# Performance work log

Measured on AMD Instinct MI355X. Metric: run time of the kernel, lower is better.

The kernel has to match this reference:

```python
import jax, jax.numpy as jnp
import numpy as np

DIM = 3072
HEADS = 24
HEAD_DIM = 128
INNER = HEADS * HEAD_DIM
EPS = 1e-6
B, IMG_LEN, TXT_LEN = 1, 2048, 512
S = IMG_LEN + TXT_LEN


def setup_inputs() -> dict:
    key = jax.random.key(0)
    ks = jax.random.split(key, 16)
    w = lambda k, shp: (jax.random.normal(k, shp, dtype=jnp.float32) * 0.02)
    return {
        "x": jax.random.normal(ks[0], (B, IMG_LEN, DIM), dtype=jnp.float32),
        "ctx": jax.random.normal(ks[1], (B, TXT_LEN, DIM), dtype=jnp.float32),
        "rope_cos": jax.random.uniform(ks[2], (S, HEAD_DIM), dtype=jnp.float32),
        "rope_sin": jax.random.uniform(ks[3], (S, HEAD_DIM), dtype=jnp.float32),
        "wq": w(ks[4], (INNER, DIM)),
        "wk": w(ks[5], (INNER, DIM)),
        "wv": w(ks[6], (INNER, DIM)),
        "gq": jnp.ones((HEAD_DIM,), jnp.float32),
        "gk": jnp.ones((HEAD_DIM,), jnp.float32),
        "wo": w(ks[7], (DIM, INNER)),
        "awq": w(ks[8], (INNER, DIM)),
        "awk": w(ks[9], (INNER, DIM)),
        "awv": w(ks[10], (INNER, DIM)),
        "agq": jnp.ones((HEAD_DIM,), jnp.float32),
        "agk": jnp.ones((HEAD_DIM,), jnp.float32),
        "awo": w(ks[11], (DIM, INNER)),
    }


def _rms_norm(t, g):
    # t: [b, s, h, d]; normalize over last dim
    var = jnp.mean(t * t, axis=-1, keepdims=True)
    return t * jax.lax.rsqrt(var + EPS) * g


def _heads(t):
    # [b, s, h*d] -> [b, s, h, d]
    b, s, _ = t.shape
    return t.reshape(b, s, HEADS, HEAD_DIM)


def _apply_rope(t, cos, sin):
    # t: [b, s, h, d]; cos/sin: [s, d] interleaved-pair layout (diffusers Flux style)
    b, s, h, d = t.shape
    x = t.reshape(b, s, h, d // 2, 2)
    rot = jnp.stack([-x[..., 1], x[..., 0]], axis=-1).reshape(b, s, h, d)
    c = cos[None, :, None, :]
    si = sin[None, :, None, :]
    return t * c + rot * si


def reference(x, ctx, rope_cos, rope_sin, wq, wk, wv, gq, gk, wo,
              awq, awk, awv, agq, agk, awo):
    # image-stream QKV + per-head RMSNorm on q,k
    q = _rms_norm(_heads(x @ wq.T), gq)
    k = _rms_norm(_heads(x @ wk.T), gk)
    v = _heads(x @ wv.T)
    # context-stream QKV
    qc = _rms_norm(_heads(ctx @ awq.T), agq)
    kc = _rms_norm(_heads(ctx @ awk.T), agk)
    vc = _heads(ctx @ awv.T)
    # joint streams: [ctx, img] ordering (out[:, :txt_len] is context)
    q = jnp.concatenate([qc, q], axis=1)
    k = jnp.concatenate([kc, k], axis=1)
    v = jnp.concatenate([vc, v], axis=1)
    q = _apply_rope(q, rope_cos, rope_sin)
    k = _apply_rope(k, rope_cos, rope_sin)
    # SDPA
    scale = 1.0 / jnp.sqrt(jnp.float32(HEAD_DIM))
    scores = jnp.einsum('bqhd,bkhd->bhqk', q, k) * scale
    probs = jax.nn.softmax(scores, axis=-1)
    out = jnp.einsum('bhqk,bkhd->bqhd', probs, v)
    out = out.reshape(out.shape[0], out.shape[1], INNER)
    img_out = out[:, TXT_LEN:] @ wo.T
    txt_out = out[:, :TXT_LEN] @ awo.T
    return (img_out, txt_out)
```

## Files before the change

kernel.cpp:

```cpp
#include <hip/hip_runtime.h>
#include <hip/hip_bf16.h>

#define DIMC 3072
#define NHEADS 24
#define HD 128
#define SEQ 2560
#define TXTLEN 512
#define IMGLEN 2048

using short8 = __attribute__((ext_vector_type(8))) short;
using f32x4  = __attribute__((ext_vector_type(4))) float;

static __device__ __forceinline__ float bf2f(unsigned short u) {
    unsigned v = ((unsigned)u) << 16;
    return __builtin_bit_cast(float, v);
}
static __device__ __forceinline__ unsigned short f2bf(float f) {
    unsigned u = __builtin_bit_cast(unsigned, f);
    return (unsigned short)((u + 0x7FFFu + ((u >> 16) & 1u)) >> 16);
}
static __device__ __forceinline__ void gload16(const void* g, void* l) {
    __builtin_amdgcn_global_load_lds((const __attribute__((address_space(1))) unsigned int*)g,
                                     (__attribute__((address_space(3))) unsigned int*)l,
                                     16, 0, 0);
}

__global__ __launch_bounds__(256)
void castk(const float* __restrict__ in, unsigned short* __restrict__ out, int n8)
{
    const int i = blockIdx.x * 256 + threadIdx.x;
    if (i >= n8) return;
    const float4 a = *reinterpret_cast<const float4*>(in + (size_t)i * 8);
    const float4 b = *reinterpret_cast<const float4*>(in + (size_t)i * 8 + 4);
    short8 o;
    o[0] = (short)f2bf(a.x); o[1] = (short)f2bf(a.y);
    o[2] = (short)f2bf(a.z); o[3] = (short)f2bf(a.w);
    o[4] = (short)f2bf(b.x); o[5] = (short)f2bf(b.y);
    o[6] = (short)f2bf(b.z); o[7] = (short)f2bf(b.w);
    *reinterpret_cast<short8*>(out + (size_t)i * 8) = o;
}

struct W8 { const float* src[8]; };
__global__ __launch_bounds__(256)
void castw(W8 a, unsigned short* __restrict__ dstbase, int n8, size_t wsz)
{
    const int i = blockIdx.x * 256 + threadIdx.x;
    if (i >= n8) return;
    const float* in = a.src[blockIdx.y];
    unsigned short* out = dstbase + (size_t)blockIdx.y * wsz;
    const float4 av = *reinterpret_cast<const float4*>(in + (size_t)i * 8);
    const float4 bv = *reinterpret_cast<const float4*>(in + (size_t)i * 8 + 4);
    short8 o;
    o[0] = (short)f2bf(av.x); o[1] = (short)f2bf(av.y);
    o[2] = (short)f2bf(av.z); o[3] = (short)f2bf(av.w);
    o[4] = (short)f2bf(bv.x); o[5] = (short)f2bf(bv.y);
    o[6] = (short)f2bf(bv.z); o[7] = (short)f2bf(bv.w);
    *reinterpret_cast<short8*>(out + (size_t)i * 8) = o;
}

struct QkvArgs {
    const unsigned short* A;
    const unsigned short* w0[3];
    const unsigned short* w1[3];
    unsigned short* c[3];
};

__global__ __launch_bounds__(256)
void gemm_qkv(QkvArgs args)
{
    __shared__ unsigned short As[2][128 * 32];
    __shared__ unsigned short Bs[2][128 * 32];

    const int bid = blockIdx.x;
    const int swz = (bid & 7) * 180 + (bid >> 3);
    const int bm = swz % 20;
    int bn = swz / 20;
    const int which = bn / 24; bn -= which * 24;

    const int rowbase = bm * 128, colbase = bn * 128;
    const unsigned short* __restrict__ A = args.A;
    const unsigned short* __restrict__ W = (rowbase < TXTLEN) ? args.w0[which] : args.w1[which];
    unsigned short* __restrict__ C = args.c[which];

    const int t = threadIdx.x, w = t >> 6, l = t & 63;
    const int lr = l & 15, lk = l >> 4;
    const int wr = (w >> 1) * 64, wc = (w & 1) * 64;

    f32x4 acc[4][4] = {};

    const unsigned short* Ag = A + (size_t)(rowbase + w * 32 + (l >> 2)) * DIMC + (l & 3) * 8;
    const unsigned short* Wg = W + (size_t)(colbase + w * 32 + (l >> 2)) * DIMC + (l & 3) * 8;

    auto STAGE = [&](int buf, int k0) {
        gload16(Ag + k0,             &As[buf][w * 1024]);
        gload16(Ag + 16 * DIMC + k0, &As[buf][w * 1024 + 512]);
        gload16(Wg + k0,             &Bs[buf][w * 1024]);
        gload16(Wg + 16 * DIMC + k0, &Bs[buf][w * 1024 + 512]);
    };

    STAGE(0, 0);

    constexpr int NIT = DIMC / 32;
    for (int it = 0; it < NIT; ++it) {
        const int buf = it & 1;
        __syncthreads();
        if (it + 1 < NIT) STAGE(buf ^ 1, (it + 1) * 32);

        short8 af[4], bf[4];
#pragma unroll
        for (int m = 0; m < 4; ++m)
            af[m] = *reinterpret_cast<const short8*>(&As[buf][(wr + m * 16 + lr) * 32 + lk * 8]);
#pragma unroll
        for (int n = 0; n < 4; ++n)
            bf[n] = *reinterpret_cast<const short8*>(&Bs[buf][(wc + n * 16 + lr) * 32 + lk * 8]);
#pragma unroll
        for (int m = 0; m < 4; ++m)
#pragma unroll
            for (int n = 0; n < 4; ++n)
                acc[m][n] = __builtin_amdgcn_mfma_f32_16x16x32_bf16(af[m], bf[n], acc[m][n], 0, 0, 0);
    }

#pragma unroll
    for (int m = 0; m < 4; ++m) {
#pragma unroll
        for (int r = 0; r < 4; ++r) {
            const int row = rowbase + wr + m * 16 + lk * 4 + r;
            unsigned short* crow = C + (size_t)row * DIMC + colbase + wc;
#pragma unroll
            for (int n = 0; n < 4; ++n)
                crow[n * 16 + lr] = f2bf(acc[m][n][r]);
        }
    }
}

__global__ __launch_bounds__(256)
void gemm_out(const unsigned short* __restrict__ A, const unsigned short* __restrict__ W0,
              const unsigned short* __restrict__ W1, float* __restrict__ Ctxt,
              float* __restrict__ Cimg)
{
    __shared__ unsigned short As[2][128 * 32];
    __shared__ unsigned short Bs[2][128 * 32];

    const int bid = blockIdx.x;
    const int swz = (bid & 7) * 60 + (bid >> 3);
    const int bm = swz % 20;
    const int bn = swz / 20;

    const int rowbase = bm * 128, colbase = bn * 128;
    const unsigned short* __restrict__ W = (rowbase < TXTLEN) ? W0 : W1;

    const int t = threadIdx.x, w = t >> 6, l = t & 63;
    const int lr = l & 15, lk = l >> 4;
    const int wr = (w >> 1) * 64, wc = (w & 1) * 64;

    f32x4 acc[4][4] = {};

    const unsigned short* Ag = A + (size_t)(rowbase + w * 32 + (l >> 2)) * DIMC + (l & 3) * 8;
    const unsigned short* Wg = W + (size_t)(colbase + w * 32 + (l >> 2)) * DIMC + (l & 3) * 8;

    auto STAGE = [&](int buf, int k0) {
        gload16(Ag + k0,             &As[buf][w * 1024]);
        gload16(Ag + 16 * DIMC + k0, &As[buf][w * 1024 + 512]);
        gload16(Wg + k0,             &Bs[buf][w * 1024]);
        gload16(Wg + 16 * DIMC + k0, &Bs[buf][w * 1024 + 512]);
    };

    STAGE(0, 0);

    constexpr int NIT = DIMC / 32;
    for (int it = 0; it < NIT; ++it) {
        const int buf = it & 1;
        __syncthreads();
        if (it + 1 < NIT) STAGE(buf ^ 1, (it + 1) * 32);

        short8 af[4], bf[4];
#pragma unroll
        for (int m = 0; m < 4; ++m)
            af[m] = *reinterpret_cast<const short8*>(&As[buf][(wr + m * 16 + lr) * 32 + lk * 8]);
#pragma unroll
        for (int n = 0; n < 4; ++n)
            bf[n] = *reinterpret_cast<const short8*>(&Bs[buf][(wc + n * 16 + lr) * 32 + lk * 8]);
#pragma unroll
        for (int m = 0; m < 4; ++m)
#pragma unroll
            for (int n = 0; n < 4; ++n)
                acc[m][n] = __builtin_amdgcn_mfma_f32_16x16x32_bf16(af[m], bf[n], acc[m][n], 0, 0, 0);
    }

    float* Cb; int rloc;
    if (rowbase < TXTLEN) { Cb = Ctxt; rloc = rowbase; }
    else                  { Cb = Cimg; rloc = rowbase - TXTLEN; }
#pragma unroll
    for (int m = 0; m < 4; ++m) {
#pragma unroll
        for (int r = 0; r < 4; ++r) {
            const int row = rloc + wr + m * 16 + lk * 4 + r;
            float* crow = Cb + (size_t)row * DIMC + colbase + wc;
#pragma unroll
            for (int n = 0; n < 4; ++n)
                crow[n * 16 + lr] = acc[m][n][r];
        }
    }
}

__global__ __launch_bounds__(256)
void normrope(unsigned short* __restrict__ Q, unsigned short* __restrict__ K,
              const float* __restrict__ gq, const float* __restrict__ gk,
              const float* __restrict__ agq, const float* __restrict__ agk,
              const float* __restrict__ rc, const float* __restrict__ rs)
{
    const int wid  = (blockIdx.x << 2) + (threadIdx.x >> 6);
    const int lane = threadIdx.x & 63;
    const int s = wid / NHEADS, h = wid - s * NHEADS;
    const bool img = (s >= TXTLEN);
    const float* gq_ = img ? gq : agq;
    const float* gk_ = img ? gk : agk;

    const size_t base = (size_t)s * DIMC + h * HD + lane * 2;
    const float2 c2  = *reinterpret_cast<const float2*>(rc + (size_t)s * HD + lane * 2);
    const float2 s2  = *reinterpret_cast<const float2*>(rs + (size_t)s * HD + lane * 2);
    const float2 gqv = *reinterpret_cast<const float2*>(gq_ + lane * 2);
    const float2 gkv = *reinterpret_cast<const float2*>(gk_ + lane * 2);

    {
        unsigned pr = *reinterpret_cast<unsigned*>(Q + base);
        float vx = bf2f((unsigned short)(pr & 0xffff));
        float vy = bf2f((unsigned short)(pr >> 16));
        float ss = vx * vx + vy * vy;
#pragma unroll
        for (int off = 1; off < 64; off <<= 1) ss += __shfl_xor(ss, off);
        const float rr = rsqrtf(ss * (1.f / HD) + 1e-6f);
        const float txv = vx * rr * gqv.x, tyv = vy * rr * gqv.y;
        const float qs = 0.08838834764831845f;
        const float ox = (txv * c2.x - tyv * s2.x) * qs;
        const float oy = (tyv * c2.y + txv * s2.y) * qs;
        *reinterpret_cast<unsigned*>(Q + base) = (unsigned)f2bf(ox) | ((unsigned)f2bf(oy) << 16);
    }
    {
        unsigned pr = *reinterpret_cast<unsigned*>(K + base);
        float vx = bf2f((unsigned short)(pr & 0xffff));
        float vy = bf2f((unsigned short)(pr >> 16));
        float ss = vx * vx + vy * vy;
#pragma unroll
        for (int off = 1; off < 64; off <<= 1) ss += __shfl_xor(ss, off);
        const float rr = rsqrtf(ss * (1.f / HD) + 1e-6f);
        const float txv = vx * rr * gkv.x, tyv = vy * rr * gkv.y;
        const float ox = txv * c2.x - tyv * s2.x;
        const float oy = tyv * c2.y + txv * s2.y;
        *reinterpret_cast<unsigned*>(K + base) = (unsigned)f2bf(ox) | ((unsigned)f2bf(oy) << 16);
    }
}

__global__ __launch_bounds__(256)
void transpose_v(const unsigned short* __restrict__ V, unsigned short* __restrict__ Vt)
{
    __shared__ unsigned short Ts[64][136];
    const int kt = blockIdx.x, h = blockIdx.y;
    const int t = threadIdx.x;
#pragma unroll
    for (int p = 0; p < 4; ++p) {
        const int row = p * 16 + (t >> 4);
        const int col = (t & 15) * 8;
        *reinterpret_cast<short8*>(&Ts[row][col]) =
            *reinterpret_cast<const short8*>(V + (size_t)(kt * 64 + row) * DIMC + h * HD + col);
    }
    __syncthreads();
    const int d = t >> 1, kh = t & 1;
    unsigned short* dst = Vt + (size_t)h * HD * SEQ + (size_t)d * SEQ + kt * 64 + kh * 32;
#pragma unroll
    for (int j4 = 0; j4 < 4; ++j4) {
        short8 o;
#pragma unroll
        for (int j = 0; j < 8; ++j) o[j] = (short)Ts[kh * 32 + j4 * 8 + j][d];
        *reinterpret_cast<short8*>(dst + j4 * 8) = o;
    }
}

__global__ __launch_bounds__(512)
void attn_mfma(const unsigned short* __restrict__ Q, const unsigned short* __restrict__ K,
               const unsigned short* __restrict__ Vt, unsigned short* __restrict__ O)
{
    __shared__ unsigned short Ks[2][64 * 128];
    __shared__ unsigned short Vs[2][128 * 64];
    __shared__ unsigned short Ps[8][16 * 64];

    const int bq = blockIdx.x, h = blockIdx.y;
    const int t = threadIdx.x, w = t >> 6, l = t & 63;
    const int lr = l & 15, lk = l >> 4;
    const int q0 = bq * 128 + w * 16;

    short8 qf[4];
#pragma unroll
    for (int kk = 0; kk < 4; ++kk)
        qf[kk] = *reinterpret_cast<const short8*>(
            Q + (size_t)(q0 + lr) * DIMC + h * HD + kk * 32 + lk * 8);

    f32x4 oacc[8] = {};
    float mrow[4] = {-1e30f, -1e30f, -1e30f, -1e30f};
    float lrow[4] = {};

    const unsigned short* Kg[2];
    const unsigned short* Vg[2];
#pragma unroll
    for (int i = 0; i < 2; ++i) {
        const int kr = w * 8 + i * 4 + (l >> 4);
        Kg[i] = K + (size_t)kr * DIMC + h * HD + (((l & 15) ^ (kr & 7)) * 8);
        const int vr = w * 16 + i * 8 + (l >> 3);
        Vg[i] = Vt + (size_t)h * HD * SEQ + (size_t)vr * SEQ + (((l & 7) ^ (vr & 7)) * 8);
    }

    auto STAGE = [&](int buf, int kv0) {
#pragma unroll
        for (int i = 0; i < 2; ++i) {
            gload16(Kg[i] + (size_t)kv0 * DIMC, &Ks[buf][(w * 8 + i * 4) * 128]);
            gload16(Vg[i] + kv0,                &Vs[buf][(w * 16 + i * 8) * 64]);
        }
    };

    STAGE(0, 0);

    constexpr int NT = SEQ / 64;
    for (int kt = 0; kt < NT; ++kt) {
        const int buf = kt & 1;
        __syncthreads();
        if (kt + 1 < NT) STAGE(buf ^ 1, (kt + 1) * 64);

        f32x4 sf[4] = {};
        __builtin_amdgcn_s_setprio(1);
#pragma unroll
        for (int nf = 0; nf < 4; ++nf) {
            const int row = nf * 16 + lr;
            const int sw = (row & 7) << 3;
#pragma unroll
            for (int kk = 0; kk < 4; ++kk) {
                short8 bfr = *reinterpret_cast<const short8*>(
                    &Ks[buf][row * 128 + ((kk * 32 + lk * 8) ^ sw)]);
                sf[nf] = __builtin_amdgcn_mfma_f32_16x16x32_bf16(qf[kk], bfr, sf[nf], 0, 0, 0);
            }
        }
        __builtin_amdgcn_s_setprio(0);

        float alpha[4];
#pragma unroll
        for (int r = 0; r < 4; ++r) {
            float mx = fmaxf(fmaxf(sf[0][r], sf[1][r]), fmaxf(sf[2][r], sf[3][r]));
#pragma unroll
            for (int off = 1; off < 16; off <<= 1) mx = fmaxf(mx, __shfl_xor(mx, off));
            const float mn = fmaxf(mrow[r], mx);
            alpha[r] = __expf(mrow[r] - mn);
            mrow[r] = mn;
            float ps = 0.f;
#pragma unroll
            for (int nf = 0; nf < 4; ++nf) {
                const float p = __expf(sf[nf][r] - mn);
                sf[nf][r] = p;
                ps += p;
            }
#pragma unroll
            for (int off = 1; off < 16; off <<= 1) ps += __shfl_xor(ps, off);
            lrow[r] = lrow[r] * alpha[r] + ps;
        }
#pragma unroll
        for (int nf = 0; nf < 8; ++nf)
#pragma unroll
            for (int r = 0; r < 4; ++r) oacc[nf][r] *= alpha[r];

#pragma unroll
        for (int r = 0; r < 4; ++r) {
            const int prow = lk * 4 + r;
            const int sw = (prow & 7) << 3;
#pragma unroll
            for (int nf = 0; nf < 4; ++nf) {
                const int col = nf * 16 + lr;
                Ps[w][prow * 64 + (col ^ sw)] = f2bf(sf[nf][r]);
            }
        }

        __builtin_amdgcn_s_setprio(1);
#pragma unroll
        for (int ks = 0; ks < 2; ++ks) {
            short8 pa = *reinterpret_cast<const short8*>(
                &Ps[w][lr * 64 + ((ks * 32 + lk * 8) ^ ((lr & 7) << 3))]);
#pragma unroll
            for (int nf = 0; nf < 8; ++nf) {
                const int vrow = nf * 16 + lr;
                short8 vf = *reinterpret_cast<const short8*>(
                    &Vs[buf][vrow * 64 + ((ks * 32 + lk * 8) ^ ((vrow & 7) << 3))]);
                oacc[nf] = __builtin_amdgcn_mfma_f32_16x16x32_bf16(pa, vf, oacc[nf], 0, 0, 0);
            }
        }
        __builtin_amdgcn_s_setprio(0);
    }

    float inv[4];
#pragma unroll
    for (int r = 0; r < 4; ++r) inv[r] = 1.f / lrow[r];
#pragma unroll
    for (int nf = 0; nf < 8; ++nf)
#pragma unroll
        for (int r = 0; r < 4; ++r)
            O[(size_t)(q0 + lk * 4 + r) * DIMC + h * HD + nf * 16 + lr] = f2bf(oacc[nf][r] * inv[r]);
}

extern "C" void kernel_launch(void* const* d_in, const int* in_sizes, int n_in,
                              void* d_out, int out_size, void* d_ws, size_t ws_size,
                              hipStream_t stream)
{
    const float* x    = (const float*)d_in[0];
    const float* ctx  = (const float*)d_in[1];
    const float* rc   = (const float*)d_in[2];
    const float* rs   = (const float*)d_in[3];
    const float* wq   = (const float*)d_in[4];
    const float* wk   = (const float*)d_in[5];
    const float* wv   = (const float*)d_in[6];
    const float* gq   = (const float*)d_in[7];
    const float* gk   = (const float*)d_in[8];
    const float* wo   = (const float*)d_in[9];
    const float* awq  = (const float*)d_in[10];
    const float* awk  = (const float*)d_in[11];
    const float* awv  = (const float*)d_in[12];
    const float* agq  = (const float*)d_in[13];
    const float* agk  = (const float*)d_in[14];
    const float* awo  = (const float*)d_in[15];

    unsigned short* wsp = (unsigned short*)d_ws;
    const size_t SZ  = (size_t)SEQ * DIMC;
    const size_t WSZ = (size_t)DIMC * DIMC;
    unsigned short* XC  = wsp;
    unsigned short* Qb  = XC + SZ;
    unsigned short* Kb  = Qb + SZ;
    unsigned short* Vb  = Kb + SZ;
    unsigned short* Vtb = Vb + SZ;
    unsigned short* Ob  = Vtb + SZ;
    unsigned short* Wc  = Ob + SZ;

    {
        int n8 = (int)((size_t)TXTLEN * DIMC / 8);
        castk<<<dim3((n8 + 255) / 256), dim3(256), 0, stream>>>(ctx, XC, n8);
        n8 = (int)((size_t)IMGLEN * DIMC / 8);
        castk<<<dim3((n8 + 255) / 256), dim3(256), 0, stream>>>(x, XC + (size_t)TXTLEN * DIMC, n8);
    }
    {
        W8 w8;
        w8.src[0] = awq; w8.src[1] = wq; w8.src[2] = awk; w8.src[3] = wk;
        w8.src[4] = awv; w8.src[5] = wv; w8.src[6] = awo; w8.src[7] = wo;
        const int n8 = (int)(WSZ / 8);
        castw<<<dim3((n8 + 255) / 256, 8), dim3(256), 0, stream>>>(w8, Wc, n8, WSZ);
    }

    QkvArgs qa;
    qa.A = XC;
    qa.w0[0] = Wc + 0 * WSZ; qa.w1[0] = Wc + 1 * WSZ; qa.c[0] = Qb;
    qa.w0[1] = Wc + 2 * WSZ; qa.w1[1] = Wc + 3 * WSZ; qa.c[1] = Kb;
    qa.w0[2] = Wc + 4 * WSZ; qa.w1[2] = Wc + 5 * WSZ; qa.c[2] = Vb;
    gemm_qkv<<<dim3(1440), dim3(256), 0, stream>>>(qa);

    normrope<<<dim3(SEQ * NHEADS / 4), dim3(256), 0, stream>>>(Qb, Kb, gq, gk, agq, agk, rc, rs);

    transpose_v<<<dim3(SEQ / 64, NHEADS), dim3(256), 0, stream>>>(Vb, Vtb);

    attn_mfma<<<dim3(SEQ / 128, NHEADS), dim3(512), 0, stream>>>(Qb, Kb, Vtb, Ob);

    float* out = (float*)d_out;
    gemm_out<<<dim3(480), dim3(256), 0, stream>>>(
        Ob, Wc + 6 * WSZ, Wc + 7 * WSZ, out + (size_t)IMGLEN * DIMC, out);
}
```

Measured before the change: 588.6 us.

## Triple-buffer GEMM prefetch and add lazy softmax rescaling in attention

```diff
diff --git a/kernel.cpp b/kernel.cpp
--- a/kernel.cpp
+++ b/kernel.cpp
@@ -68,8 +68,8 @@
 __global__ __launch_bounds__(256)
 void gemm_qkv(QkvArgs args)
 {
-    __shared__ unsigned short As[2][128 * 32];
-    __shared__ unsigned short Bs[2][128 * 32];
+    __shared__ unsigned short As[3][128 * 32];
+    __shared__ unsigned short Bs[3][128 * 32];
 
     const int bid = blockIdx.x;
     const int swz = (bid & 7) * 180 + (bid >> 3);
@@ -98,13 +98,21 @@
         gload16(Wg + 16 * DIMC + k0, &Bs[buf][w * 1024 + 512]);
     };
 
+    constexpr int NIT = DIMC / 32;
     STAGE(0, 0);
-
-    constexpr int NIT = DIMC / 32;
+    STAGE(1, 32);
+
+    int buf = 0;
     for (int it = 0; it < NIT; ++it) {
-        const int buf = it & 1;
-        __syncthreads();
-        if (it + 1 < NIT) STAGE(buf ^ 1, (it + 1) * 32);
+        asm volatile("s_waitcnt vmcnt(4)" ::: "memory");
+        __builtin_amdgcn_s_barrier();
+        asm volatile("" ::: "memory");
+
+        {
+            const int k2 = (it + 2 < NIT) ? (it + 2) : (NIT - 1);
+            int b2 = buf + 2; if (b2 >= 3) b2 -= 3;
+            STAGE(b2, k2 * 32);
+        }
 
         short8 af[4], bf[4];
 #pragma unroll
@@ -113,11 +121,16 @@
 #pragma unroll
         for (int n = 0; n < 4; ++n)
             bf[n] = *reinterpret_cast<const short8*>(&Bs[buf][(wc + n * 16 + lr) * 32 + lk * 8]);
+
+        __builtin_amdgcn_s_setprio(1);
 #pragma unroll
         for (int m = 0; m < 4; ++m)
 #pragma unroll
             for (int n = 0; n < 4; ++n)
                 acc[m][n] = __builtin_amdgcn_mfma_f32_16x16x32_bf16(af[m], bf[n], acc[m][n], 0, 0, 0);
+        __builtin_amdgcn_s_setprio(0);
+
+        buf = (buf + 1 == 3) ? 0 : buf + 1;
     }
 
 #pragma unroll
@@ -138,8 +151,8 @@
               const unsigned short* __restrict__ W1, float* __restrict__ Ctxt,
               float* __restrict__ Cimg)
 {
-    __shared__ unsigned short As[2][128 * 32];
-    __shared__ unsigned short Bs[2][128 * 32];
+    __shared__ unsigned short As[3][128 * 32];
+    __shared__ unsigned short Bs[3][128 * 32];
 
     const int bid = blockIdx.x;
     const int swz = (bid & 7) * 60 + (bid >> 3);
@@ -165,13 +178,21 @@
         gload16(Wg + 16 * DIMC + k0, &Bs[buf][w * 1024 + 512]);
     };
 
+    constexpr int NIT = DIMC / 32;
     STAGE(0, 0);
-
-    constexpr int NIT = DIMC / 32;
+    STAGE(1, 32);
+
+    int buf = 0;
     for (int it = 0; it < NIT; ++it) {
-        const int buf = it & 1;
-        __syncthreads();
-        if (it + 1 < NIT) STAGE(buf ^ 1, (it + 1) * 32);
+        asm volatile("s_waitcnt vmcnt(4)" ::: "memory");
+        __builtin_amdgcn_s_barrier();
+        asm volatile("" ::: "memory");
+
+        {
+            const int k2 = (it + 2 < NIT) ? (it + 2) : (NIT - 1);
+            int b2 = buf + 2; if (b2 >= 3) b2 -= 3;
+            STAGE(b2, k2 * 32);
+        }
 
         short8 af[4], bf[4];
 #pragma unroll
@@ -180,11 +201,16 @@
 #pragma unroll
         for (int n = 0; n < 4; ++n)
             bf[n] = *reinterpret_cast<const short8*>(&Bs[buf][(wc + n * 16 + lr) * 32 + lk * 8]);
+
+        __builtin_amdgcn_s_setprio(1);
 #pragma unroll
         for (int m = 0; m < 4; ++m)
 #pragma unroll
             for (int n = 0; n < 4; ++n)
                 acc[m][n] = __builtin_amdgcn_mfma_f32_16x16x32_bf16(af[m], bf[n], acc[m][n], 0, 0, 0);
+        __builtin_amdgcn_s_setprio(0);
+
+        buf = (buf + 1 == 3) ? 0 : buf + 1;
     }
 
     float* Cb; int rloc;
@@ -340,30 +366,40 @@
         }
         __builtin_amdgcn_s_setprio(0);
 
-        float alpha[4];
+        float mxr[4];
 #pragma unroll
         for (int r = 0; r < 4; ++r) {
             float mx = fmaxf(fmaxf(sf[0][r], sf[1][r]), fmaxf(sf[2][r], sf[3][r]));
 #pragma unroll
             for (int off = 1; off < 16; off <<= 1) mx = fmaxf(mx, __shfl_xor(mx, off));
-            const float mn = fmaxf(mrow[r], mx);
-            alpha[r] = __expf(mrow[r] - mn);
-            mrow[r] = mn;
+            mxr[r] = mx;
+        }
+        const float need = fmaxf(fmaxf(mxr[0] - mrow[0], mxr[1] - mrow[1]),
+                                 fmaxf(mxr[2] - mrow[2], mxr[3] - mrow[3]));
+        if (!__all(need <= 8.0f)) {
+#pragma unroll
+            for (int r = 0; r < 4; ++r) {
+                const float mn = fmaxf(mrow[r], mxr[r]);
+                const float alpha = __expf(mrow[r] - mn);
+                mrow[r] = mn;
+                lrow[r] *= alpha;
+#pragma unroll
+                for (int nf = 0; nf < 8; ++nf) oacc[nf][r] *= alpha;
+            }
+        }
+#pragma unroll
+        for (int r = 0; r < 4; ++r) {
             float ps = 0.f;
 #pragma unroll
             for (int nf = 0; nf < 4; ++nf) {
-                const float p = __expf(sf[nf][r] - mn);
+                const float p = __expf(sf[nf][r] - mrow[r]);
                 sf[nf][r] = p;
                 ps += p;
             }
 #pragma unroll
             for (int off = 1; off < 16; off <<= 1) ps += __shfl_xor(ps, off);
-            lrow[r] = lrow[r] * alpha[r] + ps;
-        }
-#pragma unroll
-        for (int nf = 0; nf < 8; ++nf)
-#pragma unroll
-            for (int r = 0; r < 4; ++r) oacc[nf][r] *= alpha[r];
+            lrow[r] += ps;
+        }
 
 #pragma unroll
         for (int r = 0; r < 4; ++r) {
```

New measurement: 542.8 us. -7.8%, faster.
